# Kernel optimization log

Hardware: AMD Instinct MI355X
Metric: run time of the kernel (lower is better)

## Reference

```python
import jax, jax.numpy as jnp
import numpy as np

N_NODES = 100000
N_EDGES = 1600000
IN_DIM, HID, OUT = 128, 128, 64


def setup_inputs() -> dict:
    key = jax.random.key(0)
    ks = jax.random.split(key, 8)
    x = jax.random.normal(ks[0], (N_NODES, IN_DIM), dtype=jnp.float32)
    edge_index = jax.random.randint(ks[1], (2, N_EDGES), 0, N_NODES, dtype=jnp.int64)
    # Glorot-ish init for GCNConv linear weights (stored as [in, out]).
    W1 = jax.random.normal(ks[2], (IN_DIM, HID), dtype=jnp.float32) * (1.0 / np.sqrt(IN_DIM))
    b1 = jnp.zeros((HID,), dtype=jnp.float32)
    W2 = jax.random.normal(ks[3], (HID, HID), dtype=jnp.float32) * (1.0 / np.sqrt(HID))
    b2 = jnp.zeros((HID,), dtype=jnp.float32)
    W3 = jax.random.normal(ks[4], (HID, OUT), dtype=jnp.float32) * (1.0 / np.sqrt(HID))
    b3 = jnp.zeros((OUT,), dtype=jnp.float32)
    return {"x": x, "W1": W1, "b1": b1, "W2": W2, "b2": b2,
            "W3": W3, "b3": b3, "edge_index": edge_index}


def _gcn_norm(edge_index, num_nodes):
    # GCNConv default: add self loops, symmetric normalization D^{-1/2} A D^{-1/2}.
    loops = jnp.arange(num_nodes, dtype=edge_index.dtype)
    src = jnp.concatenate([edge_index[0], loops])
    dst = jnp.concatenate([edge_index[1], loops])
    deg = jax.ops.segment_sum(jnp.ones_like(dst, dtype=jnp.float32), dst,
                              num_segments=num_nodes)
    dinv = jnp.where(deg > 0, jax.lax.rsqrt(deg), 0.0)
    norm = dinv[src] * dinv[dst]  # [E + N]
    return src, dst, norm


def _gcn_conv(h, W, b, src, dst, norm, num_nodes):
    h = h @ W                                   # transform first (PyG GCNConv)
    msg = h[src] * norm[:, None]                # gather + scale
    agg = jax.ops.segment_sum(msg, dst, num_segments=num_nodes)  # scatter-add
    return agg + b


def _dropout(h, key, p=0.5):
    keep = jax.random.bernoulli(key, 1.0 - p, h.shape)
    return jnp.where(keep, h / (1.0 - p), 0.0)


def reference(x, W1, b1, W2, b2, W3, b3, edge_index):
    num_nodes = x.shape[0]
    src, dst, norm = _gcn_norm(edge_index, num_nodes)
    kd1, kd2 = jax.random.split(jax.random.key(42))
    h = jax.nn.relu(_gcn_conv(x, W1, b1, src, dst, norm, num_nodes))
    h = _dropout(h, kd1)
    h = jax.nn.relu(_gcn_conv(h, W2, b2, src, dst, norm, num_nodes))
    h = _dropout(h, kd2)
    return _gcn_conv(h, W3, b3, src, dst, norm, num_nodes)
```

## Files before the change

### kernel.cpp

```cpp
#include <hip/hip_runtime.h>
#include <stdint.h>

#define NN 100000
#define NE 1600000

typedef float f4 __attribute__((ext_vector_type(4)));
typedef float f2 __attribute__((ext_vector_type(2)));
typedef unsigned short us4 __attribute__((ext_vector_type(4)));
typedef short s16x8 __attribute__((ext_vector_type(8)));

__device__ inline float bf2f(unsigned short u) {
  return __uint_as_float(((uint32_t)u) << 16);
}
__device__ inline unsigned short f2bf(float f) {
  uint32_t u = __float_as_uint(f);
  return (unsigned short)((u + 0x7fffu + ((u >> 16) & 1u)) >> 16);
}
__device__ inline float lo16(uint32_t q) { return __uint_as_float(q << 16); }
__device__ inline float hi16(uint32_t q) { return __uint_as_float(q & 0xffff0000u); }

__host__ __device__ inline void threefry2x32(uint32_t k0, uint32_t k1,
                                             uint32_t x0, uint32_t x1,
                                             uint32_t* y0, uint32_t* y1) {
  uint32_t ks[3] = {k0, k1, k0 ^ k1 ^ 0x1BD11BDAu};
  x0 += ks[0]; x1 += ks[1];
  const uint32_t R[2][4] = {{13u, 15u, 26u, 6u}, {17u, 29u, 16u, 24u}};
#pragma unroll
  for (int i = 0; i < 5; ++i) {
#pragma unroll
    for (int j = 0; j < 4; ++j) {
      uint32_t r = R[i & 1][j];
      x0 += x1;
      x1 = (x1 << r) | (x1 >> (32u - r));
      x1 ^= x0;
    }
    x0 += ks[(i + 1) % 3];
    x1 += ks[(i + 2) % 3] + (uint32_t)(i + 1);
  }
  *y0 = x0; *y1 = x1;
}

__device__ inline uint32_t tf_bits32(uint32_t k0, uint32_t k1, uint32_t idx) {
  uint32_t a, b;
  threefry2x32(k0, k1, 0u, idx, &a, &b);
  return a ^ b;
}

__global__ void k_init(uint32_t* cnt) {
  int i = blockIdx.x * 256 + threadIdx.x;
  if (i < NN) cnt[i] = 0u;
}

__global__ void k_hist(const int* __restrict__ ei, uint32_t* __restrict__ cnt,
                       int* __restrict__ slot) {
  int e = blockIdx.x * 256 + threadIdx.x;
  if (e < NE) {
    int d = ei[NE + e];
    slot[e] = (int)atomicAdd(&cnt[d], 1u);
  }
}

__global__ void k_dinv(const uint32_t* __restrict__ cnt, float* __restrict__ dinv) {
  int i = blockIdx.x * 256 + threadIdx.x;
  if (i < NN) dinv[i] = 1.0f / sqrtf((float)(cnt[i] + 1u));
}

__global__ __launch_bounds__(256) void k_scan1(const uint32_t* __restrict__ cnt,
                                               uint32_t* __restrict__ rp,
                                               uint32_t* __restrict__ bsum) {
  __shared__ uint32_t sh[256];
  int t = threadIdx.x;
  int base = blockIdx.x * 1024 + t * 4;
  uint32_t v[4];
  uint32_t s = 0;
#pragma unroll
  for (int i = 0; i < 4; ++i) {
    int idx = base + i;
    v[i] = (idx < NN) ? cnt[idx] : 0u;
    s += v[i];
  }
  sh[t] = s;
  __syncthreads();
  for (int off = 1; off < 256; off <<= 1) {
    uint32_t x = sh[t];
    if (t >= off) x += sh[t - off];
    __syncthreads();
    sh[t] = x;
    __syncthreads();
  }
  uint32_t run = (t > 0) ? sh[t - 1] : 0u;
  if (t == 255) bsum[blockIdx.x] = sh[255];
#pragma unroll
  for (int i = 0; i < 4; ++i) {
    int idx = base + i;
    if (idx < NN) rp[idx] = run;
    run += v[i];
  }
}

__global__ void k_scan2(uint32_t* bsum, int nb) {
  if (threadIdx.x == 0 && blockIdx.x == 0) {
    uint32_t s = 0;
    for (int i = 0; i < nb; ++i) { uint32_t x = bsum[i]; bsum[i] = s; s += x; }
  }
}

__global__ void k_scan3(uint32_t* rp, const uint32_t* __restrict__ bsum) {
  int i = blockIdx.x * 256 + threadIdx.x;
  if (i < NN) rp[i] += bsum[i >> 10];
  if (i == 0) rp[NN] = (uint32_t)NE;
}

__global__ void k_scatter(const int* __restrict__ ei,
                          const uint32_t* __restrict__ rp,
                          const int* __restrict__ slot,
                          int* __restrict__ csrc) {
  int e = blockIdx.x * 256 + threadIdx.x;
  if (e < NE) {
    int s = ei[e];
    int d = ei[NE + e];
    csrc[rp[d] + (uint32_t)slot[e]] = s;
  }
}

__global__ void k_split(const float* __restrict__ A, unsigned short* __restrict__ H,
                        unsigned short* __restrict__ L) {
  int i = blockIdx.x * 256 + threadIdx.x;
  f4 v = ((const f4*)A)[i];
  us4 h, l;
#pragma unroll
  for (int j = 0; j < 4; ++j) {
    h[j] = f2bf(v[j]);
    l[j] = f2bf(v[j] - bf2f(h[j]));
  }
  ((us4*)H)[i] = h;
  ((us4*)L)[i] = l;
}

__global__ void k_wsplit(const float* __restrict__ W, int dout,
                         unsigned short* __restrict__ H,
                         unsigned short* __restrict__ L) {
  int lane = threadIdx.x;
  int kk = blockIdx.x & 3;
  int ct = blockIdx.x >> 2;
  int kbase = kk * 32 + (lane >> 4) * 8;
  int col = ct * 16 + (lane & 15);
  us4 h0, h1, l0, l1;
#pragma unroll
  for (int j = 0; j < 4; ++j) {
    float v = W[(size_t)(kbase + j) * dout + col];
    h0[j] = f2bf(v);
    l0[j] = f2bf(v - bf2f(h0[j]));
    float v2 = W[(size_t)(kbase + 4 + j) * dout + col];
    h1[j] = f2bf(v2);
    l1[j] = f2bf(v2 - bf2f(h1[j]));
  }
  size_t o = ((size_t)blockIdx.x * 64 + lane) * 8;
  *(us4*)(H + o) = h0; *(us4*)(H + o + 4) = h1;
  *(us4*)(L + o) = l0; *(us4*)(L + o + 4) = l1;
}

template <int DOUT>
__global__ __launch_bounds__(256) void k_gemm_mfma(
    const unsigned short* __restrict__ Ah, const unsigned short* __restrict__ Al,
    const unsigned short* __restrict__ Wh, const unsigned short* __restrict__ Wl,
    unsigned short* __restrict__ C) {
  constexpr int NT = DOUT / 16;
  const int w = threadIdx.x >> 6;
  const int lane = threadIdx.x & 63;
  const int row0 = blockIdx.x * 64 + w * 16;
  int ar = row0 + (lane & 15);
  if (ar >= NN) ar = NN - 1;
  const int aoff = (lane >> 4) * 8;
  s16x8 afh[4], afl[4];
#pragma unroll
  for (int kk = 0; kk < 4; ++kk) {
    afh[kk] = *(const s16x8*)(Ah + (size_t)ar * 128 + kk * 32 + aoff);
    afl[kk] = *(const s16x8*)(Al + (size_t)ar * 128 + kk * 32 + aoff);
  }
  f4 acc[NT];
#pragma unroll
  for (int t = 0; t < NT; ++t) acc[t] = (f4){0.f, 0.f, 0.f, 0.f};
#pragma unroll
  for (int ct = 0; ct < NT; ++ct) {
#pragma unroll
    for (int kk = 0; kk < 4; ++kk) {
      size_t bo = ((size_t)(ct * 4 + kk) * 64 + lane) * 8;
      s16x8 bh = *(const s16x8*)(Wh + bo);
      s16x8 bl = *(const s16x8*)(Wl + bo);
      acc[ct] = __builtin_amdgcn_mfma_f32_16x16x32_bf16(afh[kk], bh, acc[ct], 0, 0, 0);
      acc[ct] = __builtin_amdgcn_mfma_f32_16x16x32_bf16(afh[kk], bl, acc[ct], 0, 0, 0);
      acc[ct] = __builtin_amdgcn_mfma_f32_16x16x32_bf16(afl[kk], bh, acc[ct], 0, 0, 0);
    }
  }
  const int rbase = row0 + (lane >> 4) * 4;
  const int cbase = lane & 15;
#pragma unroll
  for (int ct = 0; ct < NT; ++ct) {
#pragma unroll
    for (int r = 0; r < 4; ++r) {
      int gr = rbase + r;
      if (gr < NN) C[(size_t)gr * DOUT + ct * 16 + cbase] = f2bf(acc[ct][r]);
    }
  }
}

__global__ __launch_bounds__(256) void k_agg_mid(
    const unsigned short* __restrict__ hb, const uint32_t* __restrict__ rp,
    const int* __restrict__ csrc, const float* __restrict__ dinv,
    const float* __restrict__ bias, unsigned short* __restrict__ oh,
    unsigned short* __restrict__ ol, uint32_t k0, uint32_t k1) {
  int wid = __builtin_amdgcn_readfirstlane(blockIdx.x * 4 + (threadIdx.x >> 6));
  if (wid >= NN) return;
  const int lane = threadIdx.x & 63;
  const uint32_t beg = rp[wid], end = rp[wid + 1];
  const float dv = dinv[wid];
  const float sn = dv * dv;
  const char* hbase = (const char*)hb;
  float a0 = 0.f, a1 = 0.f, c0 = 0.f, c1 = 0.f;
  uint32_t u = beg;
  for (; u + 4 <= end; u += 4) {
    int s0 = csrc[u], s1 = csrc[u + 1], s2 = csrc[u + 2], s3 = csrc[u + 3];
    float w0 = dinv[s0] * dv, w1 = dinv[s1] * dv;
    float w2 = dinv[s2] * dv, w3 = dinv[s3] * dv;
    uint32_t q0 = ((const uint32_t*)(hbase + ((size_t)(uint32_t)s0 << 8)))[lane];
    uint32_t q1 = ((const uint32_t*)(hbase + ((size_t)(uint32_t)s1 << 8)))[lane];
    uint32_t q2 = ((const uint32_t*)(hbase + ((size_t)(uint32_t)s2 << 8)))[lane];
    uint32_t q3 = ((const uint32_t*)(hbase + ((size_t)(uint32_t)s3 << 8)))[lane];
    a0 = fmaf(w0, lo16(q0), a0); a1 = fmaf(w0, hi16(q0), a1);
    c0 = fmaf(w1, lo16(q1), c0); c1 = fmaf(w1, hi16(q1), c1);
    a0 = fmaf(w2, lo16(q2), a0); a1 = fmaf(w2, hi16(q2), a1);
    c0 = fmaf(w3, lo16(q3), c0); c1 = fmaf(w3, hi16(q3), c1);
  }
  for (; u < end; ++u) {
    int s0 = csrc[u];
    float w0 = dinv[s0] * dv;
    uint32_t q0 = ((const uint32_t*)(hbase + ((size_t)(uint32_t)s0 << 8)))[lane];
    a0 = fmaf(w0, lo16(q0), a0); a1 = fmaf(w0, hi16(q0), a1);
  }
  a0 += c0; a1 += c1;
  uint32_t qs = ((const uint32_t*)(hbase + ((size_t)(uint32_t)wid << 8)))[lane];
  f2 bv = *(const f2*)(bias + lane * 2);
  a0 = fmaf(sn, lo16(qs), a0) + bv[0];
  a1 = fmaf(sn, hi16(qs), a1) + bv[1];
  a0 = fmaxf(a0, 0.f);
  a1 = fmaxf(a1, 0.f);
  uint32_t i0 = (uint32_t)wid * 128u + (uint32_t)lane * 2u;
  uint32_t m0 = tf_bits32(k0, k1, i0);
  uint32_t m1 = tf_bits32(k0, k1, i0 + 1u);
  a0 = (m0 & 0x80000000u) ? 0.f : a0 * 2.f;
  a1 = (m1 & 0x80000000u) ? 0.f : a1 * 2.f;
  unsigned short h0 = f2bf(a0), h1 = f2bf(a1);
  unsigned short g0 = f2bf(a0 - bf2f(h0)), g1 = f2bf(a1 - bf2f(h1));
  ((uint32_t*)oh)[(size_t)wid * 64 + lane] = (uint32_t)h0 | ((uint32_t)h1 << 16);
  ((uint32_t*)ol)[(size_t)wid * 64 + lane] = (uint32_t)g0 | ((uint32_t)g1 << 16);
}

__global__ __launch_bounds__(256) void k_agg_final(
    const unsigned short* __restrict__ hb, const uint32_t* __restrict__ rp,
    const int* __restrict__ csrc, const float* __restrict__ dinv,
    const float* __restrict__ bias, float* __restrict__ out) {
  int wid = __builtin_amdgcn_readfirstlane(blockIdx.x * 4 + (threadIdx.x >> 6));
  if (wid >= NN) return;
  const int lane = threadIdx.x & 63;
  const uint32_t beg = rp[wid], end = rp[wid + 1];
  const float dv = dinv[wid];
  const float sn = dv * dv;
  const char* hbase = (const char*)hb;
  float a0 = 0.f, c0 = 0.f, a2 = 0.f, c2 = 0.f;
  uint32_t u = beg;
  for (; u + 4 <= end; u += 4) {
    int s0 = csrc[u], s1 = csrc[u + 1], s2 = csrc[u + 2], s3 = csrc[u + 3];
    float w0 = dinv[s0] * dv, w1 = dinv[s1] * dv;
    float w2 = dinv[s2] * dv, w3 = dinv[s3] * dv;
    uint32_t q0 = (uint32_t)((const unsigned short*)(hbase + ((size_t)(uint32_t)s0 << 7)))[lane];
    uint32_t q1 = (uint32_t)((const unsigned short*)(hbase + ((size_t)(uint32_t)s1 << 7)))[lane];
    uint32_t q2 = (uint32_t)((const unsigned short*)(hbase + ((size_t)(uint32_t)s2 << 7)))[lane];
    uint32_t q3 = (uint32_t)((const unsigned short*)(hbase + ((size_t)(uint32_t)s3 << 7)))[lane];
    a0 = fmaf(w0, lo16(q0), a0);
    c0 = fmaf(w1, lo16(q1), c0);
    a2 = fmaf(w2, lo16(q2), a2);
    c2 = fmaf(w3, lo16(q3), c2);
  }
  for (; u < end; ++u) {
    int s0 = csrc[u];
    float w0 = dinv[s0] * dv;
    uint32_t q0 = (uint32_t)((const unsigned short*)(hbase + ((size_t)(uint32_t)s0 << 7)))[lane];
    a0 = fmaf(w0, lo16(q0), a0);
  }
  a0 += c0 + a2 + c2;
  uint32_t qs = (uint32_t)((const unsigned short*)(hbase + ((size_t)(uint32_t)wid << 7)))[lane];
  a0 = fmaf(sn, lo16(qs), a0) + bias[lane];
  out[(size_t)wid * 64 + lane] = a0;
}

extern "C" void kernel_launch(void* const* d_in, const int* in_sizes, int n_in,
                              void* d_out, int out_size, void* d_ws, size_t ws_size,
                              hipStream_t stream) {
  (void)in_sizes; (void)n_in; (void)out_size; (void)ws_size;
  const float* x  = (const float*)d_in[0];
  const float* W1 = (const float*)d_in[1];
  const float* b1 = (const float*)d_in[2];
  const float* W2 = (const float*)d_in[3];
  const float* b2 = (const float*)d_in[4];
  const float* W3 = (const float*)d_in[5];
  const float* b3 = (const float*)d_in[6];
  const int* ei   = (const int*)d_in[7];
  float* out = (float*)d_out;

  char* p = (char*)d_ws;
  auto alloc = [&](size_t bytes) -> void* {
    void* r = (void*)p;
    p += (bytes + 255) & ~(size_t)255;
    return r;
  };
  uint32_t* cnt  = (uint32_t*)alloc((size_t)NN * 4);
  float*    dinv = (float*)alloc((size_t)NN * 4);
  uint32_t* rp   = (uint32_t*)alloc((size_t)(NN + 1) * 4);
  uint32_t* bsum = (uint32_t*)alloc(1024);
  int*      slot = (int*)alloc((size_t)NE * 4);
  int*      csrc = (int*)alloc((size_t)NE * 4);
  unsigned short* ah = (unsigned short*)alloc((size_t)NN * 128 * 2);
  unsigned short* al = (unsigned short*)alloc((size_t)NN * 128 * 2);
  unsigned short* hb = (unsigned short*)alloc((size_t)NN * 128 * 2);
  unsigned short* w1h = (unsigned short*)alloc(32 * 64 * 8 * 2);
  unsigned short* w1l = (unsigned short*)alloc(32 * 64 * 8 * 2);
  unsigned short* w2h = (unsigned short*)alloc(32 * 64 * 8 * 2);
  unsigned short* w2l = (unsigned short*)alloc(32 * 64 * 8 * 2);
  unsigned short* w3h = (unsigned short*)alloc(16 * 64 * 8 * 2);
  unsigned short* w3l = (unsigned short*)alloc(16 * 64 * 8 * 2);

  uint32_t kd1a, kd1b, kd2a, kd2b;
  threefry2x32(0u, 42u, 0u, 0u, &kd1a, &kd1b);
  threefry2x32(0u, 42u, 0u, 1u, &kd2a, &kd2b);

  const int gbN = (NN + 255) / 256;
  const int gbE = (NE + 255) / 256;
  const int gbScan = (NN + 1023) / 1024;
  const int gbGemm = (NN + 63) / 64;
  const int gbAgg = (NN + 3) / 4;

  k_init<<<gbN, 256, 0, stream>>>(cnt);
  k_hist<<<gbE, 256, 0, stream>>>(ei, cnt, slot);
  k_dinv<<<gbN, 256, 0, stream>>>(cnt, dinv);
  k_scan1<<<gbScan, 256, 0, stream>>>(cnt, rp, bsum);
  k_scan2<<<1, 64, 0, stream>>>(bsum, gbScan);
  k_scan3<<<gbN, 256, 0, stream>>>(rp, bsum);
  k_scatter<<<gbE, 256, 0, stream>>>(ei, rp, slot, csrc);

  k_split<<<(NN * 128 / 4) / 256, 256, 0, stream>>>(x, ah, al);
  k_wsplit<<<32, 64, 0, stream>>>(W1, 128, w1h, w1l);
  k_wsplit<<<32, 64, 0, stream>>>(W2, 128, w2h, w2l);
  k_wsplit<<<16, 64, 0, stream>>>(W3, 64, w3h, w3l);

  k_gemm_mfma<128><<<gbGemm, 256, 0, stream>>>(ah, al, w1h, w1l, hb);
  k_agg_mid<<<gbAgg, 256, 0, stream>>>(hb, rp, csrc, dinv, b1, ah, al, kd1a, kd1b);
  k_gemm_mfma<128><<<gbGemm, 256, 0, stream>>>(ah, al, w2h, w2l, hb);
  k_agg_mid<<<gbAgg, 256, 0, stream>>>(hb, rp, csrc, dinv, b2, ah, al, kd2a, kd2b);
  k_gemm_mfma<64><<<gbGemm, 256, 0, stream>>>(ah, al, w3h, w3l, hb);
  k_agg_final<<<gbAgg, 256, 0, stream>>>(hb, rp, csrc, dinv, b3, out);
}
```

Baseline: 418.3 us.

## Precompute edge weights and dropout bitmasks, fuse x split into first GEMM

The CSR scatter now stores (src, normalized weight) pairs, so aggregation no longer gathers dinv per edge. Dropout bits for both layers are generated in one bit-packed mask kernel instead of calling threefry twice per element inside the aggregation. The fp32-to-bf16 hi/lo split of x is folded into a dedicated first GEMM, which removes a separate pass over x. The aggregation loops are also unrolled to 8 edges. In exchange the edge array doubles in size (8 bytes per edge), and mask generation becomes its own kernel launch.

Result: slower. 440.9 us (+5.4%).

```diff
diff --git a/kernel.cpp b/kernel.cpp
--- a/kernel.cpp
+++ b/kernel.cpp
@@ -3,6 +3,7 @@
 
 #define NN 100000
 #define NE 1600000
+#define NMASKW 400000
 
 typedef float f4 __attribute__((ext_vector_type(4)));
 typedef float f2 __attribute__((ext_vector_type(2)));
@@ -44,6 +45,23 @@
   uint32_t a, b;
   threefry2x32(k0, k1, 0u, idx, &a, &b);
   return a ^ b;
+}
+
+__global__ __launch_bounds__(256) void k_mask(uint32_t* __restrict__ m1,
+                                              uint32_t* __restrict__ m2,
+                                              uint32_t k10, uint32_t k11,
+                                              uint32_t k20, uint32_t k21) {
+  int t = blockIdx.x * 256 + threadIdx.x;
+  if (t >= NMASKW) return;
+  uint32_t base = (uint32_t)t * 32u;
+  uint32_t w1 = 0, w2 = 0;
+#pragma unroll 4
+  for (int j = 0; j < 32; ++j) {
+    w1 |= (tf_bits32(k10, k11, base + j) >> 31) << j;
+    w2 |= (tf_bits32(k20, k21, base + j) >> 31) << j;
+  }
+  m1[t] = w1;
+  m2[t] = w2;
 }
 
 __global__ void k_init(uint32_t* cnt) {
@@ -114,27 +132,19 @@
 __global__ void k_scatter(const int* __restrict__ ei,
                           const uint32_t* __restrict__ rp,
                           const int* __restrict__ slot,
-                          int* __restrict__ csrc) {
+                          const float* __restrict__ dinv,
+                          uint2* __restrict__ e2) {
   int e = blockIdx.x * 256 + threadIdx.x;
   if (e < NE) {
     int s = ei[e];
     int d = ei[NE + e];
-    csrc[rp[d] + (uint32_t)slot[e]] = s;
-  }
-}
-
-__global__ void k_split(const float* __restrict__ A, unsigned short* __restrict__ H,
-                        unsigned short* __restrict__ L) {
-  int i = blockIdx.x * 256 + threadIdx.x;
-  f4 v = ((const f4*)A)[i];
-  us4 h, l;
-#pragma unroll
-  for (int j = 0; j < 4; ++j) {
-    h[j] = f2bf(v[j]);
-    l[j] = f2bf(v[j] - bf2f(h[j]));
-  }
-  ((us4*)H)[i] = h;
-  ((us4*)L)[i] = l;
+    float w = dinv[s] * dinv[d];
+    uint32_t pos = rp[d] + (uint32_t)slot[e];
+    uint2 rec;
+    rec.x = (uint32_t)s;
+    rec.y = __float_as_uint(w);
+    e2[pos] = rec;
+  }
 }
 
 __global__ void k_wsplit(const float* __restrict__ W, int dout,
@@ -158,6 +168,58 @@
   size_t o = ((size_t)blockIdx.x * 64 + lane) * 8;
   *(us4*)(H + o) = h0; *(us4*)(H + o + 4) = h1;
   *(us4*)(L + o) = l0; *(us4*)(L + o + 4) = l1;
+}
+
+__global__ __launch_bounds__(256) void k_gemm1(
+    const float* __restrict__ A, const unsigned short* __restrict__ Wh,
+    const unsigned short* __restrict__ Wl, unsigned short* __restrict__ C) {
+  constexpr int NT = 8;
+  const int w = threadIdx.x >> 6;
+  const int lane = threadIdx.x & 63;
+  const int row0 = blockIdx.x * 64 + w * 16;
+  int ar = row0 + (lane & 15);
+  if (ar >= NN) ar = NN - 1;
+  const int aoff = (lane >> 4) * 8;
+  s16x8 afh[4], afl[4];
+#pragma unroll
+  for (int kk = 0; kk < 4; ++kk) {
+    f4 v0 = *(const f4*)(A + (size_t)ar * 128 + kk * 32 + aoff);
+    f4 v1 = *(const f4*)(A + (size_t)ar * 128 + kk * 32 + aoff + 4);
+#pragma unroll
+    for (int j = 0; j < 4; ++j) {
+      unsigned short h = f2bf(v0[j]);
+      afh[kk][j] = (short)h;
+      afl[kk][j] = (short)f2bf(v0[j] - bf2f(h));
+      unsigned short h2 = f2bf(v1[j]);
+      afh[kk][j + 4] = (short)h2;
+      afl[kk][j + 4] = (short)f2bf(v1[j] - bf2f(h2));
+    }
+  }
+  f4 acc[NT];
+#pragma unroll
+  for (int t = 0; t < NT; ++t) acc[t] = (f4){0.f, 0.f, 0.f, 0.f};
+#pragma unroll
+  for (int ct = 0; ct < NT; ++ct) {
+#pragma unroll
+    for (int kk = 0; kk < 4; ++kk) {
+      size_t bo = ((size_t)(ct * 4 + kk) * 64 + lane) * 8;
+      s16x8 bh = *(const s16x8*)(Wh + bo);
+      s16x8 bl = *(const s16x8*)(Wl + bo);
+      acc[ct] = __builtin_amdgcn_mfma_f32_16x16x32_bf16(afh[kk], bh, acc[ct], 0, 0, 0);
+      acc[ct] = __builtin_amdgcn_mfma_f32_16x16x32_bf16(afh[kk], bl, acc[ct], 0, 0, 0);
+      acc[ct] = __builtin_amdgcn_mfma_f32_16x16x32_bf16(afl[kk], bh, acc[ct], 0, 0, 0);
+    }
+  }
+  const int rbase = row0 + (lane >> 4) * 4;
+  const int cbase = lane & 15;
+#pragma unroll
+  for (int ct = 0; ct < NT; ++ct) {
+#pragma unroll
+    for (int r = 0; r < 4; ++r) {
+      int gr = rbase + r;
+      if (gr < NN) C[(size_t)gr * 128 + ct * 16 + cbase] = f2bf(acc[ct][r]);
+    }
+  }
 }
 
 template <int DOUT>
@@ -207,9 +269,9 @@
 
 __global__ __launch_bounds__(256) void k_agg_mid(
     const unsigned short* __restrict__ hb, const uint32_t* __restrict__ rp,
-    const int* __restrict__ csrc, const float* __restrict__ dinv,
-    const float* __restrict__ bias, unsigned short* __restrict__ oh,
-    unsigned short* __restrict__ ol, uint32_t k0, uint32_t k1) {
+    const uint2* __restrict__ e2, const float* __restrict__ dinv,
+    const float* __restrict__ bias, const uint32_t* __restrict__ mask,
+    unsigned short* __restrict__ oh, unsigned short* __restrict__ ol) {
   int wid = __builtin_amdgcn_readfirstlane(blockIdx.x * 4 + (threadIdx.x >> 6));
   if (wid >= NN) return;
   const int lane = threadIdx.x & 63;
@@ -219,24 +281,32 @@
   const char* hbase = (const char*)hb;
   float a0 = 0.f, a1 = 0.f, c0 = 0.f, c1 = 0.f;
   uint32_t u = beg;
-  for (; u + 4 <= end; u += 4) {
-    int s0 = csrc[u], s1 = csrc[u + 1], s2 = csrc[u + 2], s3 = csrc[u + 3];
-    float w0 = dinv[s0] * dv, w1 = dinv[s1] * dv;
-    float w2 = dinv[s2] * dv, w3 = dinv[s3] * dv;
-    uint32_t q0 = ((const uint32_t*)(hbase + ((size_t)(uint32_t)s0 << 8)))[lane];
-    uint32_t q1 = ((const uint32_t*)(hbase + ((size_t)(uint32_t)s1 << 8)))[lane];
-    uint32_t q2 = ((const uint32_t*)(hbase + ((size_t)(uint32_t)s2 << 8)))[lane];
-    uint32_t q3 = ((const uint32_t*)(hbase + ((size_t)(uint32_t)s3 << 8)))[lane];
-    a0 = fmaf(w0, lo16(q0), a0); a1 = fmaf(w0, hi16(q0), a1);
-    c0 = fmaf(w1, lo16(q1), c0); c1 = fmaf(w1, hi16(q1), c1);
-    a0 = fmaf(w2, lo16(q2), a0); a1 = fmaf(w2, hi16(q2), a1);
-    c0 = fmaf(w3, lo16(q3), c0); c1 = fmaf(w3, hi16(q3), c1);
+  for (; u + 8 <= end; u += 8) {
+    uint2 r[8];
+#pragma unroll
+    for (int i = 0; i < 8; ++i) r[i] = e2[u + i];
+    uint32_t q[8];
+#pragma unroll
+    for (int i = 0; i < 8; ++i)
+      q[i] = ((const uint32_t*)(hbase + ((size_t)r[i].x << 8)))[lane];
+#pragma unroll
+    for (int i = 0; i < 8; ++i) {
+      float w = __uint_as_float(r[i].y);
+      if (i & 1) {
+        c0 = fmaf(w, lo16(q[i]), c0);
+        c1 = fmaf(w, hi16(q[i]), c1);
+      } else {
+        a0 = fmaf(w, lo16(q[i]), a0);
+        a1 = fmaf(w, hi16(q[i]), a1);
+      }
+    }
   }
   for (; u < end; ++u) {
-    int s0 = csrc[u];
-    float w0 = dinv[s0] * dv;
-    uint32_t q0 = ((const uint32_t*)(hbase + ((size_t)(uint32_t)s0 << 8)))[lane];
-    a0 = fmaf(w0, lo16(q0), a0); a1 = fmaf(w0, hi16(q0), a1);
+    uint2 r = e2[u];
+    uint32_t q = ((const uint32_t*)(hbase + ((size_t)r.x << 8)))[lane];
+    float w = __uint_as_float(r.y);
+    a0 = fmaf(w, lo16(q), a0);
+    a1 = fmaf(w, hi16(q), a1);
   }
   a0 += c0; a1 += c1;
   uint32_t qs = ((const uint32_t*)(hbase + ((size_t)(uint32_t)wid << 8)))[lane];
@@ -245,11 +315,10 @@
   a1 = fmaf(sn, hi16(qs), a1) + bv[1];
   a0 = fmaxf(a0, 0.f);
   a1 = fmaxf(a1, 0.f);
-  uint32_t i0 = (uint32_t)wid * 128u + (uint32_t)lane * 2u;
-  uint32_t m0 = tf_bits32(k0, k1, i0);
-  uint32_t m1 = tf_bits32(k0, k1, i0 + 1u);
-  a0 = (m0 & 0x80000000u) ? 0.f : a0 * 2.f;
-  a1 = (m1 & 0x80000000u) ? 0.f : a1 * 2.f;
+  uint32_t mw = mask[(uint32_t)wid * 4u + (uint32_t)(lane >> 4)];
+  uint32_t b = (uint32_t)((lane & 15) * 2);
+  a0 = ((mw >> b) & 1u) ? 0.f : a0 * 2.f;
+  a1 = ((mw >> (b + 1u)) & 1u) ? 0.f : a1 * 2.f;
   unsigned short h0 = f2bf(a0), h1 = f2bf(a1);
   unsigned short g0 = f2bf(a0 - bf2f(h0)), g1 = f2bf(a1 - bf2f(h1));
   ((uint32_t*)oh)[(size_t)wid * 64 + lane] = (uint32_t)h0 | ((uint32_t)h1 << 16);
@@ -258,7 +327,7 @@
 
 __global__ __launch_bounds__(256) void k_agg_final(
     const unsigned short* __restrict__ hb, const uint32_t* __restrict__ rp,
-    const int* __restrict__ csrc, const float* __restrict__ dinv,
+    const uint2* __restrict__ e2, const float* __restrict__ dinv,
     const float* __restrict__ bias, float* __restrict__ out) {
   int wid = __builtin_amdgcn_readfirstlane(blockIdx.x * 4 + (threadIdx.x >> 6));
   if (wid >= NN) return;
@@ -269,28 +338,32 @@
   const char* hbase = (const char*)hb;
   float a0 = 0.f, c0 = 0.f, a2 = 0.f, c2 = 0.f;
   uint32_t u = beg;
-  for (; u + 4 <= end; u += 4) {
-    int s0 = csrc[u], s1 = csrc[u + 1], s2 = csrc[u + 2], s3 = csrc[u + 3];
-    float w0 = dinv[s0] * dv, w1 = dinv[s1] * dv;
-    float w2 = dinv[s2] * dv, w3 = dinv[s3] * dv;
-    uint32_t q0 = (uint32_t)((const unsigned short*)(hbase + ((size_t)(uint32_t)s0 << 7)))[lane];
-    uint32_t q1 = (uint32_t)((const unsigned short*)(hbase + ((size_t)(uint32_t)s1 << 7)))[lane];
-    uint32_t q2 = (uint32_t)((const unsigned short*)(hbase + ((size_t)(uint32_t)s2 << 7)))[lane];
-    uint32_t q3 = (uint32_t)((const unsigned short*)(hbase + ((size_t)(uint32_t)s3 << 7)))[lane];
-    a0 = fmaf(w0, lo16(q0), a0);
-    c0 = fmaf(w1, lo16(q1), c0);
-    a2 = fmaf(w2, lo16(q2), a2);
-    c2 = fmaf(w3, lo16(q3), c2);
+  for (; u + 8 <= end; u += 8) {
+    uint2 r[8];
+#pragma unroll
+    for (int i = 0; i < 8; ++i) r[i] = e2[u + i];
+    uint32_t q[8];
+#pragma unroll
+    for (int i = 0; i < 8; ++i)
+      q[i] = (uint32_t)((const unsigned short*)(hbase + ((size_t)r[i].x << 7)))[lane];
+#pragma unroll
+    for (int i = 0; i < 8; ++i) {
+      float w = __uint_as_float(r[i].y);
+      float hv = __uint_as_float(q[i] << 16);
+      if ((i & 3) == 0) a0 = fmaf(w, hv, a0);
+      else if ((i & 3) == 1) c0 = fmaf(w, hv, c0);
+      else if ((i & 3) == 2) a2 = fmaf(w, hv, a2);
+      else c2 = fmaf(w, hv, c2);
+    }
   }
   for (; u < end; ++u) {
-    int s0 = csrc[u];
-    float w0 = dinv[s0] * dv;
-    uint32_t q0 = (uint32_t)((const unsigned short*)(hbase + ((size_t)(uint32_t)s0 << 7)))[lane];
-    a0 = fmaf(w0, lo16(q0), a0);
+    uint2 r = e2[u];
+    uint32_t q = (uint32_t)((const unsigned short*)(hbase + ((size_t)r.x << 7)))[lane];
+    a0 = fmaf(__uint_as_float(r.y), __uint_as_float(q << 16), a0);
   }
   a0 += c0 + a2 + c2;
   uint32_t qs = (uint32_t)((const unsigned short*)(hbase + ((size_t)(uint32_t)wid << 7)))[lane];
-  a0 = fmaf(sn, lo16(qs), a0) + bias[lane];
+  a0 = fmaf(sn, __uint_as_float(qs << 16), a0) + bias[lane];
   out[(size_t)wid * 64 + lane] = a0;
 }
 
@@ -319,7 +392,9 @@
   uint32_t* rp   = (uint32_t*)alloc((size_t)(NN + 1) * 4);
   uint32_t* bsum = (uint32_t*)alloc(1024);
   int*      slot = (int*)alloc((size_t)NE * 4);
-  int*      csrc = (int*)alloc((size_t)NE * 4);
+  uint2*    e2   = (uint2*)alloc((size_t)NE * 8);
+  uint32_t* m1   = (uint32_t*)alloc((size_t)NMASKW * 4);
+  uint32_t* m2   = (uint32_t*)alloc((size_t)NMASKW * 4);
   unsigned short* ah = (unsigned short*)alloc((size_t)NN * 128 * 2);
   unsigned short* al = (unsigned short*)alloc((size_t)NN * 128 * 2);
   unsigned short* hb = (unsigned short*)alloc((size_t)NN * 128 * 2);
@@ -339,6 +414,7 @@
   const int gbScan = (NN + 1023) / 1024;
   const int gbGemm = (NN + 63) / 64;
   const int gbAgg = (NN + 3) / 4;
+  const int gbMask = (NMASKW + 255) / 256;
 
   k_init<<<gbN, 256, 0, stream>>>(cnt);
   k_hist<<<gbE, 256, 0, stream>>>(ei, cnt, slot);
@@ -346,17 +422,17 @@
   k_scan1<<<gbScan, 256, 0, stream>>>(cnt, rp, bsum);
   k_scan2<<<1, 64, 0, stream>>>(bsum, gbScan);
   k_scan3<<<gbN, 256, 0, stream>>>(rp, bsum);
-  k_scatter<<<gbE, 256, 0, stream>>>(ei, rp, slot, csrc);
-
-  k_split<<<(NN * 128 / 4) / 256, 256, 0, stream>>>(x, ah, al);
+  k_scatter<<<gbE, 256, 0, stream>>>(ei, rp, slot, dinv, e2);
+
+  k_mask<<<gbMask, 256, 0, stream>>>(m1, m2, kd1a, kd1b, kd2a, kd2b);
   k_wsplit<<<32, 64, 0, stream>>>(W1, 128, w1h, w1l);
   k_wsplit<<<32, 64, 0, stream>>>(W2, 128, w2h, w2l);
   k_wsplit<<<16, 64, 0, stream>>>(W3, 64, w3h, w3l);
 
-  k_gemm_mfma<128><<<gbGemm, 256, 0, stream>>>(ah, al, w1h, w1l, hb);
-  k_agg_mid<<<gbAgg, 256, 0, stream>>>(hb, rp, csrc, dinv, b1, ah, al, kd1a, kd1b);
+  k_gemm1<<<gbGemm, 256, 0, stream>>>(x, w1h, w1l, hb);
+  k_agg_mid<<<gbAgg, 256, 0, stream>>>(hb, rp, e2, dinv, b1, m1, ah, al);
   k_gemm_mfma<128><<<gbGemm, 256, 0, stream>>>(ah, al, w2h, w2l, hb);
-  k_agg_mid<<<gbAgg, 256, 0, stream>>>(hb, rp, csrc, dinv, b2, ah, al, kd2a, kd2b);
+  k_agg_mid<<<gbAgg, 256, 0, stream>>>(hb, rp, e2, dinv, b2, m2, ah, al);
   k_gemm_mfma<64><<<gbGemm, 256, 0, stream>>>(ah, al, w3h, w3l, hb);
-  k_agg_final<<<gbAgg, 256, 0, stream>>>(hb, rp, csrc, dinv, b3, out);
-}
+  k_agg_final<<<gbAgg, 256, 0, stream>>>(hb, rp, e2, dinv, b3, out);
+}
```
